# Performance work log

Measured on AMD Instinct MI355X. Metric: run time of the kernel, lower is better.

Reference implementation:

```python
import jax, jax.numpy as jnp
import numpy as np

B, S, D, H, C = 2, 2048, 1024, 16, 64

def setup_inputs() -> dict:
    key = jax.random.key(0)
    kx, kq, kk, kv, ko = jax.random.split(key, 5)
    scale = 0.02
    return {
        "x": jax.random.normal(kx, (B, S, D), dtype=jnp.float32),
        "Wq": jax.random.normal(kq, (D, H, C), dtype=jnp.float32) * scale,
        "Wk": jax.random.normal(kk, (D, H, C), dtype=jnp.float32) * scale,
        "Wv": jax.random.normal(kv, (D, H, C), dtype=jnp.float32) * scale,
        "Wo": jax.random.normal(ko, (H, C, D), dtype=jnp.float32) * scale,
    }

def reference(x, Wq, Wk, Wv, Wo):
    # project to per-head q/k/v: [B,S,H,C]
    q = jnp.einsum('bqd,dhc->bqhc', x, Wq)
    k = jnp.einsum('bkd,dhc->bkhc', x, Wk)
    v = jnp.einsum('bkd,dhc->bkhc', x, Wv)
    q = q * (C ** -0.5)
    alphas = jnp.einsum('bqhc,bkhc->bhqk', q, k)  # [B,H,S,S]
    weights = jax.nn.softmax(alphas, axis=-1)
    out = jnp.einsum('bhqk,bkhc->bqhc', weights, v)
    return jnp.einsum('bqhc,hcd->bqd', out, Wo)
```

## Files before the change

kernel.cpp:

```cpp
#include <hip/hip_runtime.h>
#include <hip/hip_bf16.h>
#include <stdint.h>
#include <stddef.h>

typedef __bf16 bf16;
typedef __bf16 bf16x4 __attribute__((ext_vector_type(4)));
typedef __bf16 bf16x8 __attribute__((ext_vector_type(8)));
typedef float f32x4 __attribute__((ext_vector_type(4)));

#define DEV __device__ __forceinline__

DEV void async16(const bf16* g, bf16* l) {
    __builtin_amdgcn_global_load_lds(
        (const __attribute__((address_space(1))) void*)g,
        (__attribute__((address_space(3))) void*)l,
        16, 0, 0);
}

DEV uint32_t pktrunc(float lo, float hi) {
    return __builtin_amdgcn_perm(__builtin_bit_cast(uint32_t, hi),
                                 __builtin_bit_cast(uint32_t, lo), 0x07060302u);
}


__global__ void prep(const float* __restrict__ x,
                     const float* __restrict__ Wq, const float* __restrict__ Wk,
                     const float* __restrict__ Wv, const float* __restrict__ Wo,
                     bf16* __restrict__ xb, bf16* __restrict__ WqkvT,
                     bf16* __restrict__ WoT) {
    __shared__ float t[32][33];
    if (blockIdx.z == 4) {
        const int bid = blockIdx.y * 32 + blockIdx.x;
#pragma unroll
        for (int i = 0; i < 4; ++i) {
            const int idx = ((bid * 4 + i) * 256 + threadIdx.x) * 4;
            const float4 v = *(const float4*)(x + idx);
            bf16 o4[4] = {(bf16)v.x, (bf16)v.y, (bf16)v.z, (bf16)v.w};
            *(uint2*)(xb + idx) = *(const uint2*)o4;
        }
        return;
    }
    const float* src;
    bf16* dst;
    float scale = 1.0f;
    switch (blockIdx.z) {
        case 0: src = Wq; dst = WqkvT; scale = 0.125f * 1.4426950408889634f; break;
        case 1: src = Wk; dst = WqkvT + 1024 * 1024; break;
        case 2: src = Wv; dst = WqkvT + 2 * 1024 * 1024; break;
        default: src = Wo; dst = WoT; break;
    }
    const int c0 = blockIdx.x * 32, r0 = blockIdx.y * 32;
    const int tx = threadIdx.x & 31, ty = threadIdx.x >> 5;
#pragma unroll
    for (int i = 0; i < 32; i += 8)
        t[ty + i][tx] = src[(size_t)(r0 + ty + i) * 1024 + c0 + tx];
    __syncthreads();
#pragma unroll
    for (int i = 0; i < 32; i += 8)
        dst[(size_t)(c0 + ty + i) * 1024 + r0 + tx] = (bf16)(t[tx][ty + i] * scale);
}


template <bool OUT_F32>
__global__ __launch_bounds__(256, 3) void gemm_bt(
    const bf16* __restrict__ A, const bf16* __restrict__ BT, void* __restrict__ Cout,
    int M, int N, int K, bf16* __restrict__ VTout) {
    __shared__ __attribute__((aligned(16))) bf16 As[2 * 128 * 32];
    __shared__ __attribute__((aligned(16))) bf16 Bs[2 * 128 * 32];
    const int tid = threadIdx.x;
    const int wid = tid >> 6;
    const int lane = tid & 63;
    const int quad = lane >> 4;
    const int l16 = lane & 15;
    const int wm = wid >> 1, wn = wid & 1;
    const int m0 = blockIdx.y * 128, n0 = blockIdx.x * 128;

    const int srow = wid * 32 + (lane >> 2);
    const int skcol = (lane & 3) * 8;
    const bf16* ag = A + (size_t)(m0 + srow) * K + skcol;
    const bf16* bg = BT + (size_t)(n0 + srow) * K + skcol;

    f32x4 acc[4][4];
#pragma unroll
    for (int i = 0; i < 4; ++i)
#pragma unroll
        for (int j = 0; j < 4; ++j) acc[i][j] = (f32x4){0.f, 0.f, 0.f, 0.f};

    for (int k0 = 0; k0 < K; k0 += 64) {
#pragma unroll
        for (int p = 0; p < 2; ++p) {
            async16(ag + k0 + p * 32, &As[p * 4096 + (wid * 32) * 32]);
            async16(ag + (size_t)16 * K + k0 + p * 32, &As[p * 4096 + (wid * 32 + 16) * 32]);
            async16(bg + k0 + p * 32, &Bs[p * 4096 + (wid * 32) * 32]);
            async16(bg + (size_t)16 * K + k0 + p * 32, &Bs[p * 4096 + (wid * 32 + 16) * 32]);
        }
        __syncthreads();

#pragma unroll
        for (int ks = 0; ks < 2; ++ks) {
            bf16x8 af[4], bfr[4];
#pragma unroll
            for (int mi = 0; mi < 4; ++mi)
                af[mi] = *(const bf16x8*)&As[ks * 4096 + (wm * 64 + mi * 16 + l16) * 32 + quad * 8];
#pragma unroll
            for (int ni = 0; ni < 4; ++ni)
                bfr[ni] = *(const bf16x8*)&Bs[ks * 4096 + (wn * 64 + ni * 16 + l16) * 32 + quad * 8];
#pragma unroll
            for (int mi = 0; mi < 4; ++mi)
#pragma unroll
                for (int ni = 0; ni < 4; ++ni)
                    acc[mi][ni] = __builtin_amdgcn_mfma_f32_16x16x32_bf16(
                        af[mi], bfr[ni], acc[mi][ni], 0, 0, 0);
        }
        __syncthreads();
    }

    if (VTout && n0 >= 2048) {
#pragma unroll
        for (int mi = 0; mi < 4; ++mi)
#pragma unroll
            for (int ni = 0; ni < 4; ++ni) {
                bf16 pk[4] = {(bf16)acc[mi][ni][0], (bf16)acc[mi][ni][1],
                              (bf16)acc[mi][ni][2], (bf16)acc[mi][ni][3]};
                *(uint2*)&VTout[(size_t)(n0 - 2048 + wn * 64 + ni * 16 + l16) * 4096 +
                                (m0 + wm * 64 + mi * 16 + quad * 4)] = *(const uint2*)pk;
            }
        return;
    }
    if (OUT_F32) {
        float* C = (float*)Cout;
#pragma unroll
        for (int mi = 0; mi < 4; ++mi)
#pragma unroll
            for (int ni = 0; ni < 4; ++ni)
#pragma unroll
                for (int r = 0; r < 4; ++r)
                    C[(size_t)(m0 + wm * 64 + mi * 16 + quad * 4 + r) * N +
                      (n0 + wn * 64 + ni * 16 + l16)] = acc[mi][ni][r];
    } else {
        bf16* C = (bf16*)Cout;
#pragma unroll
        for (int mi = 0; mi < 4; ++mi)
#pragma unroll
            for (int ni = 0; ni < 4; ++ni)
#pragma unroll
                for (int r = 0; r < 4; ++r)
                    C[(size_t)(m0 + wm * 64 + mi * 16 + quad * 4 + r) * N +
                      (n0 + wn * 64 + ni * 16 + l16)] = (bf16)acc[mi][ni][r];
    }
}


__global__ __launch_bounds__(256, 4) void gemm_tm2(
    const bf16* __restrict__ A, const bf16* __restrict__ BT, float* __restrict__ C,
    int M, int N, int K) {
    __shared__ __attribute__((aligned(16))) bf16 As[2 * 64 * 32];
    __shared__ __attribute__((aligned(16))) bf16 Bs[2 * 128 * 32];
    const int tid = threadIdx.x;
    const int wid = tid >> 6;
    const int lane = tid & 63;
    const int quad = lane >> 4;
    const int l16 = lane & 15;
    const int wm = wid >> 1, wn = wid & 1;
    const int m0 = blockIdx.y * 64, n0 = blockIdx.x * 128;

    const int srowA = wid * 16 + (lane >> 2);
    const int srowB = wid * 32 + (lane >> 2);
    const int skcol = (lane & 3) * 8;
    const bf16* ag = A + (size_t)(m0 + srowA) * K + skcol;
    const bf16* bg = BT + (size_t)(n0 + srowB) * K + skcol;

    f32x4 acc[2][4];
#pragma unroll
    for (int i = 0; i < 2; ++i)
#pragma unroll
        for (int j = 0; j < 4; ++j) acc[i][j] = (f32x4){0.f, 0.f, 0.f, 0.f};

    for (int k0 = 0; k0 < K; k0 += 64) {
#pragma unroll
        for (int p = 0; p < 2; ++p) {
            async16(ag + k0 + p * 32, &As[p * 2048 + (wid * 16) * 32]);
            async16(bg + k0 + p * 32, &Bs[p * 4096 + (wid * 32) * 32]);
            async16(bg + (size_t)16 * K + k0 + p * 32, &Bs[p * 4096 + (wid * 32 + 16) * 32]);
        }
        __syncthreads();

#pragma unroll
        for (int ks = 0; ks < 2; ++ks) {
            bf16x8 af[2], bfr[4];
#pragma unroll
            for (int mi = 0; mi < 2; ++mi)
                af[mi] = *(const bf16x8*)&As[ks * 2048 + (wm * 32 + mi * 16 + l16) * 32 + quad * 8];
#pragma unroll
            for (int ni = 0; ni < 4; ++ni)
                bfr[ni] = *(const bf16x8*)&Bs[ks * 4096 + (wn * 64 + ni * 16 + l16) * 32 + quad * 8];
#pragma unroll
            for (int mi = 0; mi < 2; ++mi)
#pragma unroll
                for (int ni = 0; ni < 4; ++ni)
                    acc[mi][ni] = __builtin_amdgcn_mfma_f32_16x16x32_bf16(
                        af[mi], bfr[ni], acc[mi][ni], 0, 0, 0);
        }
        __syncthreads();
    }

#pragma unroll
    for (int mi = 0; mi < 2; ++mi)
#pragma unroll
        for (int ni = 0; ni < 4; ++ni)
#pragma unroll
            for (int r = 0; r < 4; ++r)
                C[(size_t)(m0 + wm * 32 + mi * 16 + quad * 4 + r) * N +
                  (n0 + wn * 64 + ni * 16 + l16)] = acc[mi][ni][r];
}


__global__ __launch_bounds__(512, 4) void flash_attn(
    const bf16* __restrict__ QKV, const bf16* __restrict__ VT, bf16* __restrict__ att) {
    constexpr int LDK = 72;
    constexpr int LDV = 136;
    __shared__ __attribute__((aligned(16))) char smem[36864];
    bf16* Ks = (bf16*)smem;
    bf16* Vs = (bf16*)(smem + 18432);
    float* Osc = (float*)smem;
    float* Lred = (float*)(smem + 32768);

    const int tid = threadIdx.x, wid = tid >> 6, lane = tid & 63;
    const int quad = lane >> 4, l16 = lane & 15;
    const int qh = wid >> 1, kh = wid & 1;
    const int bh = blockIdx.x, qt = blockIdx.y;
    const int b = bh >> 4, h = bh & 15;
    const int q0 = qt * 128;

    bf16x8 qf[2][2];
    {
        const bf16* qbase = QKV + (size_t)(b * 2048 + q0 + qh * 32 + l16) * 3072 + h * 64 + quad * 8;
#pragma unroll
        for (int mi = 0; mi < 2; ++mi)
#pragma unroll
            for (int ks = 0; ks < 2; ++ks)
                qf[mi][ks] = *(const bf16x8*)(qbase + (size_t)mi * 16 * 3072 + ks * 32);
    }

    const int krow = tid >> 3, kcol = (tid & 7) * 8;
    const int vrow = tid >> 4, vcol = (tid & 15) * 8;
    const bf16* kg = QKV + (size_t)(b * 2048 + krow) * 3072 + 1024 + h * 64 + kcol;
    const bf16* vg = VT + (size_t)(h * 64 + vrow) * 4096 + b * 2048 + vcol;

    bf16x8 kr[2], vr[2];
#pragma unroll
    for (int p = 0; p < 2; ++p) {
        kr[p] = *(const bf16x8*)(kg + (size_t)(64 * p) * 3072);
        vr[p] = *(const bf16x8*)(vg + (size_t)(32 * p) * 4096);
    }

    const bf16 one = (bf16)1.0f;
    const bf16x8 onesf = (bf16x8){one, one, one, one, one, one, one, one};

    f32x4 o[2][4];
    f32x4 ls[2];
#pragma unroll
    for (int mi = 0; mi < 2; ++mi) {
        ls[mi] = (f32x4){0.f, 0.f, 0.f, 0.f};
#pragma unroll
        for (int ct = 0; ct < 4; ++ct) o[mi][ct] = (f32x4){0.f, 0.f, 0.f, 0.f};
    }

    for (int it = 0; it < 16; ++it) {
#pragma unroll
        for (int p = 0; p < 2; ++p) {
            *(bf16x8*)&Ks[(64 * p + krow) * LDK + kcol] = kr[p];
            *(bf16x8*)&Vs[(32 * p + vrow) * LDV + vcol] = vr[p];
        }
        __syncthreads();

        if (it < 15) {
            const size_t ko = (size_t)(it + 1) * 128;
#pragma unroll
            for (int p = 0; p < 2; ++p) {
                kr[p] = *(const bf16x8*)(kg + (ko + 64 * p) * 3072);
                vr[p] = *(const bf16x8*)(vg + (size_t)(32 * p) * 4096 + ko);
            }
        }

#pragma unroll
        for (int pr = 0; pr < 2; ++pr) {
            const int kb = kh * 64 + pr * 32;
            const bf16x8 kfA0 = *(const bf16x8*)&Ks[(kb + l16) * LDK + quad * 8];
            const bf16x8 kfA1 = *(const bf16x8*)&Ks[(kb + l16) * LDK + 32 + quad * 8];
            const bf16x8 kfB0 = *(const bf16x8*)&Ks[(kb + 16 + l16) * LDK + quad * 8];
            const bf16x8 kfB1 = *(const bf16x8*)&Ks[(kb + 16 + l16) * LDK + 32 + quad * 8];
            bf16x8 vf[4];
#pragma unroll
            for (int ct = 0; ct < 4; ++ct) {
                const bf16x4 lo = *(const bf16x4*)&Vs[(ct * 16 + l16) * LDV + kb + quad * 4];
                const bf16x4 hi = *(const bf16x4*)&Vs[(ct * 16 + l16) * LDV + kb + 16 + quad * 4];
                vf[ct] = (bf16x8){lo[0], lo[1], lo[2], lo[3], hi[0], hi[1], hi[2], hi[3]};
            }
#pragma unroll
            for (int mi = 0; mi < 2; ++mi) {
                f32x4 sA = (f32x4){0.f, 0.f, 0.f, 0.f};
                f32x4 sB = (f32x4){0.f, 0.f, 0.f, 0.f};
                sA = __builtin_amdgcn_mfma_f32_16x16x32_bf16(kfA0, qf[mi][0], sA, 0, 0, 0);
                sA = __builtin_amdgcn_mfma_f32_16x16x32_bf16(kfA1, qf[mi][1], sA, 0, 0, 0);
                sB = __builtin_amdgcn_mfma_f32_16x16x32_bf16(kfB0, qf[mi][0], sB, 0, 0, 0);
                sB = __builtin_amdgcn_mfma_f32_16x16x32_bf16(kfB1, qf[mi][1], sB, 0, 0, 0);

                const float pa0 = __builtin_amdgcn_exp2f(sA[0]);
                const float pa1 = __builtin_amdgcn_exp2f(sA[1]);
                const float pa2 = __builtin_amdgcn_exp2f(sA[2]);
                const float pa3 = __builtin_amdgcn_exp2f(sA[3]);
                const float pb0 = __builtin_amdgcn_exp2f(sB[0]);
                const float pb1 = __builtin_amdgcn_exp2f(sB[1]);
                const float pb2 = __builtin_amdgcn_exp2f(sB[2]);
                const float pb3 = __builtin_amdgcn_exp2f(sB[3]);

                union { uint32_t u[4]; bf16x8 v; } pu;
                pu.u[0] = pktrunc(pa0, pa1);
                pu.u[1] = pktrunc(pa2, pa3);
                pu.u[2] = pktrunc(pb0, pb1);
                pu.u[3] = pktrunc(pb2, pb3);
                const bf16x8 pf = pu.v;
#pragma unroll
                for (int ct = 0; ct < 4; ++ct)
                    o[mi][ct] = __builtin_amdgcn_mfma_f32_16x16x32_bf16(pf, vf[ct], o[mi][ct], 0, 0, 0);
                ls[mi] = __builtin_amdgcn_mfma_f32_16x16x32_bf16(pf, onesf, ls[mi], 0, 0, 0);
            }
        }
        __syncthreads();
    }

    if (l16 == 0) {
#pragma unroll
        for (int mi = 0; mi < 2; ++mi)
#pragma unroll
            for (int r = 0; r < 4; ++r)
                Lred[wid * 32 + mi * 16 + quad * 4 + r] = ls[mi][r];
    }
    if (kh == 1) {
        float* dst = Osc + qh * 2048;
#pragma unroll
        for (int mi = 0; mi < 2; ++mi)
#pragma unroll
            for (int ct = 0; ct < 4; ++ct)
                *(f32x4*)(dst + (mi * 4 + ct) * 256 + lane * 4) = o[mi][ct];
    }
    __syncthreads();

    if (kh == 0) {
        const float* src = Osc + qh * 2048;
#pragma unroll
        for (int mi = 0; mi < 2; ++mi)
#pragma unroll
            for (int ct = 0; ct < 4; ++ct)
                o[mi][ct] += *(const f32x4*)(src + (mi * 4 + ct) * 256 + lane * 4);
#pragma unroll
        for (int mi = 0; mi < 2; ++mi)
#pragma unroll
            for (int r = 0; r < 4; ++r) {
                const int qrow = mi * 16 + quad * 4 + r;
                const float l = Lred[(qh * 2) * 32 + qrow] + Lred[(qh * 2 + 1) * 32 + qrow];
                const float inv = 1.0f / l;
                bf16* orow = att + (size_t)(b * 2048 + q0 + qh * 32 + qrow) * 1024 + h * 64 + l16;
#pragma unroll
                for (int ct = 0; ct < 4; ++ct)
                    orow[ct * 16] = (bf16)(o[mi][ct][r] * inv);
            }
    }
}


extern "C" void kernel_launch(void* const* d_in, const int* in_sizes, int n_in,
                              void* d_out, int out_size, void* d_ws, size_t ws_size,
                              hipStream_t stream) {
    (void)in_sizes; (void)n_in; (void)out_size; (void)ws_size;
    const float* x  = (const float*)d_in[0];
    const float* Wq = (const float*)d_in[1];
    const float* Wk = (const float*)d_in[2];
    const float* Wv = (const float*)d_in[3];
    const float* Wo = (const float*)d_in[4];

    char* ws = (char*)d_ws;
    bf16* xb    = (bf16*)(ws);
    bf16* att   = xb;
    bf16* WqkvT = (bf16*)(ws + (size_t)8  * 1024 * 1024);
    bf16* WoT   = (bf16*)(ws + (size_t)14 * 1024 * 1024);
    bf16* QKV   = (bf16*)(ws + (size_t)16 * 1024 * 1024);
    bf16* VT    = (bf16*)(ws + (size_t)40 * 1024 * 1024);

    prep<<<dim3(32, 32, 5), 256, 0, stream>>>(x, Wq, Wk, Wv, Wo, xb, WqkvT, WoT);

    gemm_bt<false><<<dim3(3072 / 128, 4096 / 128), 256, 0, stream>>>(
        xb, WqkvT, QKV, 4096, 3072, 1024, VT);

    flash_attn<<<dim3(32, 16), 512, 0, stream>>>(QKV, VT, att);

    gemm_tm2<<<dim3(1024 / 128, 4096 / 64), 256, 0, stream>>>(
        att, WoT, (float*)d_out, 4096, 1024, 1024);
}
```

Measured before the change: 181.9 us.

## Load V fragments directly from global and double-buffer K in LDS

V tiles are no longer staged through shared memory. Each wave now reads its V MFMA operands straight from global memory (the transposed VT buffer) as 8-byte loads. K staging becomes double-buffered in LDS, which removes the second barrier per iteration. The aim is to cut LDS traffic and synchronisation. In exchange, the V loads are narrow and redundant across waves, and their global latency now sits in the inner compute loop.

```diff
diff --git a/kernel.cpp b/kernel.cpp
--- a/kernel.cpp
+++ b/kernel.cpp
@@ -218,12 +218,10 @@
 __global__ __launch_bounds__(512, 4) void flash_attn(
     const bf16* __restrict__ QKV, const bf16* __restrict__ VT, bf16* __restrict__ att) {
     constexpr int LDK = 72;
-    constexpr int LDV = 136;
-    __shared__ __attribute__((aligned(16))) char smem[36864];
-    bf16* Ks = (bf16*)smem;
-    bf16* Vs = (bf16*)(smem + 18432);
+    constexpr int KBUF = 128 * LDK * 2;
+    __shared__ __attribute__((aligned(16))) char smem[2 * KBUF + 1024];
     float* Osc = (float*)smem;
-    float* Lred = (float*)(smem + 32768);
+    float* Lred = (float*)(smem + 2 * KBUF);
 
     const int tid = threadIdx.x, wid = tid >> 6, lane = tid & 63;
     const int quad = lane >> 4, l16 = lane & 15;
@@ -243,16 +241,13 @@
     }
 
     const int krow = tid >> 3, kcol = (tid & 7) * 8;
-    const int vrow = tid >> 4, vcol = (tid & 15) * 8;
     const bf16* kg = QKV + (size_t)(b * 2048 + krow) * 3072 + 1024 + h * 64 + kcol;
-    const bf16* vg = VT + (size_t)(h * 64 + vrow) * 4096 + b * 2048 + vcol;
-
-    bf16x8 kr[2], vr[2];
-#pragma unroll
-    for (int p = 0; p < 2; ++p) {
+    const bf16* vg = VT + (size_t)(h * 64 + l16) * 4096 + b * 2048 + quad * 4;
+
+    bf16x8 kr[2];
+#pragma unroll
+    for (int p = 0; p < 2; ++p)
         kr[p] = *(const bf16x8*)(kg + (size_t)(64 * p) * 3072);
-        vr[p] = *(const bf16x8*)(vg + (size_t)(32 * p) * 4096);
-    }
 
     const bf16 one = (bf16)1.0f;
     const bf16x8 onesf = (bf16x8){one, one, one, one, one, one, one, one};
@@ -267,36 +262,34 @@
     }
 
     for (int it = 0; it < 16; ++it) {
-#pragma unroll
-        for (int p = 0; p < 2; ++p) {
+        bf16* Ks = (bf16*)(smem + (it & 1) * KBUF);
+
+#pragma unroll
+        for (int p = 0; p < 2; ++p)
             *(bf16x8*)&Ks[(64 * p + krow) * LDK + kcol] = kr[p];
-            *(bf16x8*)&Vs[(32 * p + vrow) * LDV + vcol] = vr[p];
-        }
         __syncthreads();
 
         if (it < 15) {
             const size_t ko = (size_t)(it + 1) * 128;
 #pragma unroll
-            for (int p = 0; p < 2; ++p) {
+            for (int p = 0; p < 2; ++p)
                 kr[p] = *(const bf16x8*)(kg + (ko + 64 * p) * 3072);
-                vr[p] = *(const bf16x8*)(vg + (size_t)(32 * p) * 4096 + ko);
-            }
         }
 
 #pragma unroll
         for (int pr = 0; pr < 2; ++pr) {
             const int kb = kh * 64 + pr * 32;
+            bf16x4 vlo[4], vhi[4];
+#pragma unroll
+            for (int ct = 0; ct < 4; ++ct) {
+                const bf16* vp = vg + (size_t)(ct * 16) * 4096 + it * 128 + kb;
+                vlo[ct] = *(const bf16x4*)vp;
+                vhi[ct] = *(const bf16x4*)(vp + 16);
+            }
             const bf16x8 kfA0 = *(const bf16x8*)&Ks[(kb + l16) * LDK + quad * 8];
             const bf16x8 kfA1 = *(const bf16x8*)&Ks[(kb + l16) * LDK + 32 + quad * 8];
             const bf16x8 kfB0 = *(const bf16x8*)&Ks[(kb + 16 + l16) * LDK + quad * 8];
             const bf16x8 kfB1 = *(const bf16x8*)&Ks[(kb + 16 + l16) * LDK + 32 + quad * 8];
-            bf16x8 vf[4];
-#pragma unroll
-            for (int ct = 0; ct < 4; ++ct) {
-                const bf16x4 lo = *(const bf16x4*)&Vs[(ct * 16 + l16) * LDV + kb + quad * 4];
-                const bf16x4 hi = *(const bf16x4*)&Vs[(ct * 16 + l16) * LDV + kb + 16 + quad * 4];
-                vf[ct] = (bf16x8){lo[0], lo[1], lo[2], lo[3], hi[0], hi[1], hi[2], hi[3]};
-            }
 #pragma unroll
             for (int mi = 0; mi < 2; ++mi) {
                 f32x4 sA = (f32x4){0.f, 0.f, 0.f, 0.f};
@@ -322,13 +315,16 @@
                 pu.u[3] = pktrunc(pb2, pb3);
                 const bf16x8 pf = pu.v;
 #pragma unroll
-                for (int ct = 0; ct < 4; ++ct)
-                    o[mi][ct] = __builtin_amdgcn_mfma_f32_16x16x32_bf16(pf, vf[ct], o[mi][ct], 0, 0, 0);
+                for (int ct = 0; ct < 4; ++ct) {
+                    const bf16x8 vf = (bf16x8){vlo[ct][0], vlo[ct][1], vlo[ct][2], vlo[ct][3],
+                                               vhi[ct][0], vhi[ct][1], vhi[ct][2], vhi[ct][3]};
+                    o[mi][ct] = __builtin_amdgcn_mfma_f32_16x16x32_bf16(pf, vf, o[mi][ct], 0, 0, 0);
+                }
                 ls[mi] = __builtin_amdgcn_mfma_f32_16x16x32_bf16(pf, onesf, ls[mi], 0, 0, 0);
             }
         }
-        __syncthreads();
-    }
+    }
+    __syncthreads();
 
     if (l16 == 0) {
 #pragma unroll
```

Result: slower. 263.4 us (+44.8%).
